# Kernel tuning notes

Measured on AMD Instinct MI355X. Metric: run time of the kernel, lower is better.

## Reference

```python
import jax, jax.numpy as jnp
import numpy as np

N_NODES = 50000
N_EDGES = 800000
NODE_DIM = 8
EDGE_DIM = 3
HIDDEN = 256
EMBED = 256
HEADS = 4
HEAD_DIM = HIDDEN // HEADS
LAYERS = 3
NUM_GRAPHS = 64
NEG_SLOPE = 0.2


def layer_norm(x, g, b, eps=1e-5):
    mu = jnp.mean(x, axis=-1, keepdims=True)
    var = jnp.var(x, axis=-1, keepdims=True)
    return (x - mu) * jax.lax.rsqrt(var + eps) * g + b


def setup_inputs() -> dict:
    key = jax.random.key(0)
    ks = jax.random.split(key, 20)
    s = lambda d: 1.0 / np.sqrt(d)
    inp = {
        "x": jax.random.normal(ks[0], (N_NODES, NODE_DIM), jnp.float32),
        "edge_index": jax.random.randint(ks[1], (2, N_EDGES), 0, N_NODES, jnp.int64),
        "edge_attr": jax.random.normal(ks[2], (N_EDGES, EDGE_DIM), jnp.float32),
        "batch": jnp.sort(jax.random.randint(ks[3], (N_NODES,), 0, NUM_GRAPHS, jnp.int64)),
        # input projection + LayerNorm
        "W_in": jax.random.normal(ks[4], (NODE_DIM, HIDDEN), jnp.float32) * s(NODE_DIM),
        "b_in": jnp.zeros((HIDDEN,), jnp.float32),
        "ln_in_g": jnp.ones((HIDDEN,), jnp.float32),
        "ln_in_b": jnp.zeros((HIDDEN,), jnp.float32),
        # stacked GAT layer params [LAYERS, ...]
        "W_gat": jax.random.normal(ks[5], (LAYERS, HIDDEN, HIDDEN), jnp.float32) * s(HIDDEN),
        "b_gat": jnp.zeros((LAYERS, HIDDEN), jnp.float32),
        "W_e": jax.random.normal(ks[6], (LAYERS, EDGE_DIM, HIDDEN), jnp.float32) * s(EDGE_DIM),
        "a_src": jax.random.normal(ks[7], (LAYERS, HEADS, HEAD_DIM), jnp.float32) * s(HEAD_DIM),
        "a_dst": jax.random.normal(ks[8], (LAYERS, HEADS, HEAD_DIM), jnp.float32) * s(HEAD_DIM),
        "a_edge": jax.random.normal(ks[9], (LAYERS, HEADS, HEAD_DIM), jnp.float32) * s(HEAD_DIM),
        # output projection + LayerNorm
        "W_out": jax.random.normal(ks[10], (EMBED, EMBED), jnp.float32) * s(EMBED),
        "b_out": jnp.zeros((EMBED,), jnp.float32),
        "ln_out_g": jnp.ones((EMBED,), jnp.float32),
        "ln_out_b": jnp.zeros((EMBED,), jnp.float32),
    }
    return inp


def gat_layer(h, src, dst, edge_attr, W, b, We, a_s, a_d, a_e):
    N = h.shape[0]
    hp = (h @ W + b).reshape(N, HEADS, HEAD_DIM)                 # [N,H,D]
    ep = (edge_attr @ We).reshape(-1, HEADS, HEAD_DIM)           # [E,H,D]
    hs = hp[src]                                                 # [E,H,D] gather
    hd = hp[dst]
    logit = (hs * a_s).sum(-1) + (hd * a_d).sum(-1) + (ep * a_e).sum(-1)  # [E,H]
    logit = jax.nn.leaky_relu(logit, NEG_SLOPE)
    # segment softmax over incoming edges per destination node
    m = jax.ops.segment_max(logit, dst, num_segments=N)          # [N,H]
    m = jnp.where(jnp.isfinite(m), m, 0.0)
    ex = jnp.exp(logit - m[dst])
    denom = jax.ops.segment_sum(ex, dst, num_segments=N)         # [N,H]
    alpha = ex / jnp.maximum(denom[dst], 1e-16)                  # [E,H]
    msg = hs * alpha[:, :, None]                                 # [E,H,D]
    out = jax.ops.segment_sum(msg, dst, num_segments=N).reshape(N, HIDDEN)
    return jax.nn.elu(out + h)                                   # residual + activation


def reference(x, edge_index, edge_attr, batch, W_in, b_in, ln_in_g, ln_in_b,
              W_gat, b_gat, W_e, a_src, a_dst, a_edge,
              W_out, b_out, ln_out_g, ln_out_b):
    src, dst = edge_index[0], edge_index[1]
    h = jax.nn.elu(layer_norm(x @ W_in + b_in, ln_in_g, ln_in_b))
    for l in range(LAYERS):
        h = gat_layer(h, src, dst, edge_attr,
                      W_gat[l], b_gat[l], W_e[l], a_src[l], a_dst[l], a_edge[l])
    node_emb = jax.nn.elu(layer_norm(h @ W_out + b_out, ln_out_g, ln_out_b))
    # global mean pool per graph
    sums = jax.ops.segment_sum(node_emb, batch, num_segments=NUM_GRAPHS)
    cnt = jax.ops.segment_sum(jnp.ones((node_emb.shape[0],), node_emb.dtype), batch,
                              num_segments=NUM_GRAPHS)
    graph_emb = sums / jnp.maximum(cnt, 1.0)[:, None]
    return graph_emb, node_emb
```

## Files before the change

### kernel.cpp

```cpp
#include <hip/hip_runtime.h>
#include <math.h>

#define HIDDEN 256
#define HEADS 4
#define HEAD_DIM 64
#define LAYERS 3
#define NUM_GRAPHS 64
#define NEG_SLOPE 0.2f

typedef short short8 __attribute__((ext_vector_type(8)));
typedef float floatx4 __attribute__((ext_vector_type(4)));

static __device__ __forceinline__ float elu_f(float x) {
    return x > 0.f ? x : expm1f(x);
}

static __device__ __forceinline__ float waveReduceSum(float v) {
#pragma unroll
    for (int off = 32; off > 0; off >>= 1) v += __shfl_xor(v, off, 64);
    return v;
}

static __device__ __forceinline__ ushort f2bf(float f) {
    unsigned u = __float_as_uint(f);
    unsigned r = (u + 0x7FFFu + ((u >> 16) & 1u)) >> 16;
    return (ushort)r;
}
static __device__ __forceinline__ float bf2f(ushort h) {
    return __uint_as_float(((unsigned)h) << 16);
}

__global__ void hist_kernel(const int* __restrict__ dst, int* __restrict__ deg, int E) {
    int e = blockIdx.x * blockDim.x + threadIdx.x;
    if (e < E) atomicAdd(&deg[dst[e]], 1);
}

__global__ __launch_bounds__(256) void blocksum_kernel(const int* __restrict__ deg,
                                                       int* __restrict__ bsum, int N) {
    int i = blockIdx.x * 256 + threadIdx.x;
    int v = (i < N) ? deg[i] : 0;
    __shared__ int red[4];
    int s = v;
#pragma unroll
    for (int off = 32; off > 0; off >>= 1) s += __shfl_xor(s, off, 64);
    if ((threadIdx.x & 63) == 0) red[threadIdx.x >> 6] = s;
    __syncthreads();
    if (threadIdx.x == 0) bsum[blockIdx.x] = red[0] + red[1] + red[2] + red[3];
}

__global__ __launch_bounds__(256) void scan_bsums(int* __restrict__ bsum, int nblk) {
    __shared__ int sh[256];
    int t = threadIdx.x;
    int v = (t < nblk) ? bsum[t] : 0;
    sh[t] = v;
    __syncthreads();
#pragma unroll
    for (int off = 1; off < 256; off <<= 1) {
        int add = (t >= off) ? sh[t - off] : 0;
        __syncthreads();
        sh[t] += add;
        __syncthreads();
    }
    if (t < nblk) bsum[t] = sh[t] - v;
}

__global__ __launch_bounds__(256) void writeptr_kernel(const int* __restrict__ deg,
                                                       const int* __restrict__ bsum,
                                                       int* __restrict__ rowptr,
                                                       int* __restrict__ nxt,
                                                       int N, int E) {
    __shared__ int sh[256];
    int t = threadIdx.x;
    int i = blockIdx.x * 256 + t;
    int v = (i < N) ? deg[i] : 0;
    sh[t] = v;
    __syncthreads();
#pragma unroll
    for (int off = 1; off < 256; off <<= 1) {
        int add = (t >= off) ? sh[t - off] : 0;
        __syncthreads();
        sh[t] += add;
        __syncthreads();
    }
    if (i < N) {
        int r = bsum[blockIdx.x] + sh[t] - v;
        rowptr[i] = r;
        nxt[i] = r;
    }
    if (i == 0) rowptr[N] = E;
}

__global__ void scatter_kernel(const int* __restrict__ src, const int* __restrict__ dst,
                               const float* __restrict__ ea, const float* __restrict__ wea,
                               int* __restrict__ nxt, int* __restrict__ smeta,
                               float* __restrict__ esc0, float* __restrict__ esc1,
                               float* __restrict__ esc2, int E) {
    int e = blockIdx.x * blockDim.x + threadIdx.x;
    if (e >= E) return;
    int d = dst[e];
    int slot = atomicAdd(&nxt[d], 1);
    smeta[slot] = src[e];
    float e0 = ea[(size_t)e * 3], e1 = ea[(size_t)e * 3 + 1], e2 = ea[(size_t)e * 3 + 2];
    float* escs[3] = {esc0, esc1, esc2};
#pragma unroll
    for (int l = 0; l < 3; ++l) {
        float4 v;
        float* vp = (float*)&v;
#pragma unroll
        for (int h = 0; h < 4; ++h) {
            const float* w = wea + l * 12 + h * 3;
            vp[h] = e0 * w[0] + e1 * w[1] + e2 * w[2];
        }
        *(float4*)(escs[l] + (size_t)slot * 4) = v;
    }
}

__global__ void wea_kernel(const float* __restrict__ We, const float* __restrict__ a_e,
                           float* __restrict__ w_ea) {
    int t = threadIdx.x;
    if (t < LAYERS * HEADS * 3) {
        int l = t / 12, r = t % 12, h = r / 3, k = r % 3;
        float s = 0.f;
        for (int d = 0; d < HEAD_DIM; ++d)
            s += We[l * 3 * HIDDEN + k * HIDDEN + h * HEAD_DIM + d] *
                 a_e[l * HIDDEN + h * HEAD_DIM + d];
        w_ea[t] = s;
    }
}

__global__ void conv_w(const float* __restrict__ Wg, const float* __restrict__ Wo,
                       ushort* __restrict__ Wt) {
    int l = blockIdx.x;
    int n = blockIdx.y;
    int k = threadIdx.x;
    const float* W = (l < 3) ? (Wg + (size_t)l * HIDDEN * HIDDEN) : Wo;
    Wt[(size_t)l * HIDDEN * HIDDEN + (size_t)n * HIDDEN + k] =
        f2bf(W[(size_t)k * HIDDEN + n]);
}

__global__ __launch_bounds__(256) void inproj_ln(const float* __restrict__ x,
                                                 const float* __restrict__ W,
                                                 const float* __restrict__ b,
                                                 const float* __restrict__ g,
                                                 const float* __restrict__ beta,
                                                 float* __restrict__ h,
                                                 ushort* __restrict__ hb) {
    int n = blockIdx.x;
    int c = threadIdx.x;
    float acc = b[c];
#pragma unroll
    for (int k = 0; k < 8; ++k) acc += x[n * 8 + k] * W[k * HIDDEN + c];
    __shared__ float red[8];
    float s = waveReduceSum(acc);
    float s2 = waveReduceSum(acc * acc);
    int w = c >> 6;
    if ((c & 63) == 0) { red[w] = s; red[4 + w] = s2; }
    __syncthreads();
    float mu = (red[0] + red[1] + red[2] + red[3]) * (1.f / 256.f);
    float ms = (red[4] + red[5] + red[6] + red[7]) * (1.f / 256.f);
    float inv = rsqrtf(ms - mu * mu + 1e-5f);
    float y = elu_f((acc - mu) * inv * g[c] + beta[c]);
    h[(size_t)n * HIDDEN + c] = y;
    hb[(size_t)n * HIDDEN + c] = f2bf(y);
}

__global__ __launch_bounds__(256) void ln_elu(const float* __restrict__ t,
                                              const float* __restrict__ g,
                                              const float* __restrict__ beta,
                                              float* __restrict__ out) {
    int n = blockIdx.x;
    int c = threadIdx.x;
    float acc = t[(size_t)n * HIDDEN + c];
    __shared__ float red[8];
    float s = waveReduceSum(acc);
    float s2 = waveReduceSum(acc * acc);
    int w = c >> 6;
    if ((c & 63) == 0) { red[w] = s; red[4 + w] = s2; }
    __syncthreads();
    float mu = (red[0] + red[1] + red[2] + red[3]) * (1.f / 256.f);
    float ms = (red[4] + red[5] + red[6] + red[7]) * (1.f / 256.f);
    float inv = rsqrtf(ms - mu * mu + 1e-5f);
    float y = (acc - mu) * inv * g[c] + beta[c];
    out[(size_t)n * HIDDEN + c] = elu_f(y);
}

#define ASTR 40
__global__ __launch_bounds__(256) void gemm_mfma(const ushort* __restrict__ A,
                                                 const ushort* __restrict__ Bt,
                                                 const float* __restrict__ bias,
                                                 float* __restrict__ C32,
                                                 ushort* __restrict__ C16,
                                                 const float* __restrict__ a_s,
                                                 const float* __restrict__ a_d,
                                                 float* __restrict__ s_src,
                                                 float* __restrict__ s_dst,
                                                 int doScore) {
    const int K = 256;
    __shared__ ushort As[128 * ASTR];
    __shared__ ushort Bs[128 * ASTR];
    int m0 = blockIdx.x * 128;
    int n0 = blockIdx.y * 128;
    int t = threadIdx.x;
    int wave = t >> 6, lane = t & 63;
    int wr = wave >> 1, wc = wave & 1;
    int lrow = lane & 15;
    int quad = lane >> 4;
    floatx4 acc[4][4] = {};
    int r = t >> 2, q = t & 3;
    for (int k0 = 0; k0 < K; k0 += 32) {
        __syncthreads();
        *(uint4*)&As[(r) * ASTR + q * 8] =
            *(const uint4*)(A + (size_t)(m0 + r) * K + k0 + q * 8);
        *(uint4*)&As[(r + 64) * ASTR + q * 8] =
            *(const uint4*)(A + (size_t)(m0 + r + 64) * K + k0 + q * 8);
        *(uint4*)&Bs[(r) * ASTR + q * 8] =
            *(const uint4*)(Bt + (size_t)(n0 + r) * K + k0 + q * 8);
        *(uint4*)&Bs[(r + 64) * ASTR + q * 8] =
            *(const uint4*)(Bt + (size_t)(n0 + r + 64) * K + k0 + q * 8);
        __syncthreads();
        short8 af[4], bfr[4];
#pragma unroll
        for (int i = 0; i < 4; ++i)
            af[i] = *(const short8*)&As[(wr * 64 + i * 16 + lrow) * ASTR + quad * 8];
#pragma unroll
        for (int j = 0; j < 4; ++j)
            bfr[j] = *(const short8*)&Bs[(wc * 64 + j * 16 + lrow) * ASTR + quad * 8];
#pragma unroll
        for (int i = 0; i < 4; ++i)
#pragma unroll
            for (int j = 0; j < 4; ++j)
                acc[i][j] = __builtin_amdgcn_mfma_f32_16x16x32_bf16(af[i], bfr[j],
                                                                    acc[i][j], 0, 0, 0);
    }
    int hh = (n0 + wc * 64) >> 6;
    int ncol[4];
    float bv4[4], asv[4], adv[4];
#pragma unroll
    for (int j = 0; j < 4; ++j) {
        int n = n0 + wc * 64 + j * 16 + lrow;
        ncol[j] = n;
        bv4[j] = bias[n];
        asv[j] = a_s[n];
        adv[j] = a_d[n];
    }
#pragma unroll
    for (int i = 0; i < 4; ++i) {
#pragma unroll
        for (int rg = 0; rg < 4; ++rg) {
            int mrow = m0 + wr * 64 + i * 16 + quad * 4 + rg;
            float ps = 0.f, pd = 0.f;
#pragma unroll
            for (int j = 0; j < 4; ++j) {
                float v = acc[i][j][rg] + bv4[j];
                if (C32) C32[(size_t)mrow * HIDDEN + ncol[j]] = v;
                if (C16) C16[(size_t)mrow * HIDDEN + ncol[j]] = f2bf(v);
                ps = fmaf(v, asv[j], ps);
                pd = fmaf(v, adv[j], pd);
            }
            if (doScore) {
#pragma unroll
                for (int off = 1; off < 16; off <<= 1) {
                    ps += __shfl_xor(ps, off, 64);
                    pd += __shfl_xor(pd, off, 64);
                }
                if (lrow == 0) {
                    s_src[mrow * 4 + hh] = ps;
                    s_dst[mrow * 4 + hh] = pd;
                }
            }
        }
    }
}

__global__ __launch_bounds__(256) void aggregate(const int* __restrict__ rowptr,
                                                 const int* __restrict__ smeta,
                                                 const float* __restrict__ escl,
                                                 const float* __restrict__ s_src,
                                                 const float* __restrict__ s_dst,
                                                 const ushort* __restrict__ hpb,
                                                 const float* __restrict__ h_in,
                                                 float* __restrict__ h_out,
                                                 ushort* __restrict__ h_out_bf,
                                                 int N) {
    int wv = threadIdx.x >> 6;
    int n = blockIdx.x * 4 + wv;
    if (n >= N) return;
    int l = threadIdx.x & 63;
    int h = l >> 4;
    int e4 = l & 15;
    int c0 = l * 4;
    float sdn = s_dst[n * 4 + h];
    int beg = rowptr[n];
    int cnt = rowptr[n + 1] - beg;
    float m = -3e38f, dsum = 0.f, a0 = 0.f, a1 = 0.f, a2 = 0.f, a3 = 0.f;
    for (int ch = 0; ch < cnt; ch += 16) {
        int i = ch + e4;
        int s = 0;
        float lg = -3e38f;
        if (i < cnt) {
            s = smeta[beg + i];
            float tv = sdn + s_src[s * 4 + h] + escl[(size_t)(beg + i) * 4 + h];
            lg = tv > 0.f ? tv : NEG_SLOPE * tv;
        }
        float cm = lg;
#pragma unroll
        for (int off = 1; off < 16; off <<= 1)
            cm = fmaxf(cm, __shfl_xor(cm, off, 64));
        float mn = fmaxf(m, cm);
        float scl = __expf(m - mn);
        m = mn;
        dsum *= scl; a0 *= scl; a1 *= scl; a2 *= scl; a3 *= scl;
        float ex = __expf(lg - mn);
        int lim = min(16, cnt - ch);
#pragma unroll 4
        for (int j = 0; j < lim; ++j) {
            float exj = __shfl(ex, (h << 4) | j, 64);
            int sj = __shfl(s, j, 64);
            uint2 v = *(const uint2*)(hpb + (size_t)sj * HIDDEN + c0);
            dsum += exj;
            float f0 = __uint_as_float(v.x << 16);
            float f1 = __uint_as_float(v.x & 0xFFFF0000u);
            float f2 = __uint_as_float(v.y << 16);
            float f3 = __uint_as_float(v.y & 0xFFFF0000u);
            a0 = fmaf(f0, exj, a0);
            a1 = fmaf(f1, exj, a1);
            a2 = fmaf(f2, exj, a2);
            a3 = fmaf(f3, exj, a3);
        }
    }
    float inv = 1.f / fmaxf(dsum, 1e-16f);
    float4 hi = *(const float4*)(h_in + (size_t)n * HIDDEN + c0);
    float y0 = elu_f(fmaf(a0, inv, hi.x));
    float y1 = elu_f(fmaf(a1, inv, hi.y));
    float y2 = elu_f(fmaf(a2, inv, hi.z));
    float y3 = elu_f(fmaf(a3, inv, hi.w));
    float4 yo = {y0, y1, y2, y3};
    *(float4*)(h_out + (size_t)n * HIDDEN + c0) = yo;
    ushort4 yb = {f2bf(y0), f2bf(y1), f2bf(y2), f2bf(y3)};
    *(ushort4*)(h_out_bf + (size_t)n * HIDDEN + c0) = yb;
}

__global__ __launch_bounds__(256) void pool_partial(const float* __restrict__ nemb,
                                                    const int* __restrict__ batch,
                                                    float* __restrict__ gout, int N) {
    int r0 = blockIdx.x * 128;
    int c = threadIdx.x;
    __shared__ int bsh[128];
    if (c < 128) {
        int r = r0 + c;
        bsh[c] = (r < N) ? batch[r] : -1;
    }
    __syncthreads();
    int rend = min(128, N - r0);
    float acc = 0.f;
    int cur = bsh[0];
    for (int i = 0; i < rend; ++i) {
        int g = bsh[i];
        if (g != cur) {
            atomicAdd(&gout[cur * HIDDEN + c], acc);
            acc = 0.f;
            cur = g;
        }
        acc += nemb[(size_t)(r0 + i) * HIDDEN + c];
    }
    if (cur >= 0) atomicAdd(&gout[cur * HIDDEN + c], acc);
}

__global__ void pool_div(float* __restrict__ gout, const int* __restrict__ batch, int N) {
    int g = blockIdx.x;
    int c = threadIdx.x;
    int lo = 0, hi = N;
    while (lo < hi) { int mid = (lo + hi) >> 1; if (batch[mid] < g) lo = mid + 1; else hi = mid; }
    int start = lo;
    lo = start; hi = N;
    while (lo < hi) { int mid = (lo + hi) >> 1; if (batch[mid] < g + 1) lo = mid + 1; else hi = mid; }
    float cnt = (float)(lo - start);
    gout[g * HIDDEN + c] /= fmaxf(cnt, 1.f);
}

extern "C" void kernel_launch(void* const* d_in, const int* in_sizes, int n_in,
                              void* d_out, int out_size, void* d_ws, size_t ws_size,
                              hipStream_t stream) {
    const float* x       = (const float*)d_in[0];
    const int*   ei      = (const int*)d_in[1];
    const float* ea      = (const float*)d_in[2];
    const int*   batch   = (const int*)d_in[3];
    const float* W_in    = (const float*)d_in[4];
    const float* b_in    = (const float*)d_in[5];
    const float* ln_in_g = (const float*)d_in[6];
    const float* ln_in_b = (const float*)d_in[7];
    const float* W_gat   = (const float*)d_in[8];
    const float* b_gat   = (const float*)d_in[9];
    const float* W_e     = (const float*)d_in[10];
    const float* a_src   = (const float*)d_in[11];
    const float* a_dst   = (const float*)d_in[12];
    const float* a_edge  = (const float*)d_in[13];
    const float* W_out   = (const float*)d_in[14];
    const float* b_out   = (const float*)d_in[15];
    const float* ln_out_g= (const float*)d_in[16];
    const float* ln_out_b= (const float*)d_in[17];

    int N = in_sizes[0] / 8;
    int E = in_sizes[1] / 2;
    int Mpad = (N + 127) & ~127;
    int nblk = (N + 255) / 256;
    const int* srcA = ei;
    const int* dstA = ei + E;

    char* w = (char*)d_ws;
    size_t off = 0;
    auto alloc = [&](size_t bytes) {
        void* p = w + off;
        off += (bytes + 255) & ~(size_t)255;
        return p;
    };
    float*    hA     = (float*)alloc((size_t)Mpad * HIDDEN * 4);
    float*    hB     = (float*)alloc((size_t)Mpad * HIDDEN * 4);
    ushort*   hAb    = (ushort*)alloc((size_t)Mpad * HIDDEN * 2);
    ushort*   hBb    = (ushort*)alloc((size_t)Mpad * HIDDEN * 2);
    ushort*   hpb    = (ushort*)alloc((size_t)Mpad * HIDDEN * 2);
    float*    sSrc   = (float*)alloc((size_t)Mpad * 4 * 4);
    float*    sDst   = (float*)alloc((size_t)Mpad * 4 * 4);
    int*      deg    = (int*)alloc((size_t)N * 4);
    int*      rowptr = (int*)alloc((size_t)(N + 1) * 4);
    int*      nxt    = (int*)alloc((size_t)N * 4);
    int*      bsum   = (int*)alloc(256 * 4);
    int*      smeta  = (int*)alloc((size_t)E * 4);
    float*    esc0   = (float*)alloc((size_t)E * 4 * 4);
    float*    esc1   = (float*)alloc((size_t)E * 4 * 4);
    float*    esc2   = (float*)alloc((size_t)E * 4 * 4);
    float*    wea    = (float*)alloc(64 * 4);
    ushort*   Wt     = (ushort*)alloc((size_t)4 * HIDDEN * HIDDEN * 2);
    float*    escs[3] = {esc0, esc1, esc2};

    hipMemsetAsync(deg, 0, (size_t)N * 4, stream);
    hist_kernel<<<(E + 255) / 256, 256, 0, stream>>>(dstA, deg, E);
    blocksum_kernel<<<nblk, 256, 0, stream>>>(deg, bsum, N);
    scan_bsums<<<1, 256, 0, stream>>>(bsum, nblk);
    writeptr_kernel<<<nblk, 256, 0, stream>>>(deg, bsum, rowptr, nxt, N, E);
    wea_kernel<<<1, 64, 0, stream>>>(W_e, a_edge, wea);
    scatter_kernel<<<(E + 255) / 256, 256, 0, stream>>>(srcA, dstA, ea, wea, nxt,
                                                        smeta, esc0, esc1, esc2, E);
    conv_w<<<dim3(4, HIDDEN), 256, 0, stream>>>(W_gat, W_out, Wt);

    inproj_ln<<<N, 256, 0, stream>>>(x, W_in, b_in, ln_in_g, ln_in_b, hA, hAb);

    float* hcur = hA;   ushort* hcurb = hAb;
    float* hnext = hB;  ushort* hnextb = hBb;
    dim3 gg(Mpad / 128, HIDDEN / 128);
    for (int l = 0; l < LAYERS; ++l) {
        gemm_mfma<<<gg, 256, 0, stream>>>(hcurb, Wt + (size_t)l * HIDDEN * HIDDEN,
                                          b_gat + l * HIDDEN, nullptr, hpb,
                                          a_src + l * HIDDEN, a_dst + l * HIDDEN,
                                          sSrc, sDst, 1);
        aggregate<<<(N + 3) / 4, 256, 0, stream>>>(rowptr, smeta, escs[l], sSrc, sDst,
                                                   hpb, hcur, hnext, hnextb, N);
        float* tf = hcur; hcur = hnext; hnext = tf;
        ushort* tb = hcurb; hcurb = hnextb; hnextb = tb;
    }

    float* hp32 = hnext;
    gemm_mfma<<<gg, 256, 0, stream>>>(hcurb, Wt + (size_t)3 * HIDDEN * HIDDEN,
                                      b_out, hp32, nullptr, a_src, a_dst, sSrc, sDst, 0);
    float* gout = (float*)d_out;
    float* nemb = gout + (size_t)NUM_GRAPHS * HIDDEN;
    ln_elu<<<N, 256, 0, stream>>>(hp32, ln_out_g, ln_out_b, nemb);
    hipMemsetAsync(gout, 0, (size_t)NUM_GRAPHS * HIDDEN * 4, stream);
    pool_partial<<<(N + 127) / 128, 256, 0, stream>>>(nemb, batch, gout, N);
    pool_div<<<NUM_GRAPHS, 256, 0, stream>>>(gout, batch, N);
}
```

Measured before the change: 749.5 us.

## Pack edge metadata and recompute edge scores; register-prefetch GEMM tiles

The scatter kernel now writes one packed 16-byte record per edge (source index plus three raw edge attributes) instead of a source index and three per-layer score arrays. Each aggregate call recomputes the per-head edge score from those attributes and the layer's folded edge weights. This cuts scatter write traffic, though aggregate now reads 16 bytes per edge instead of 4+4 (a slot in a 16-byte record). Separately, the GEMM prefetches the next K-slice into registers while the current slice is computed, overlapping global loads with MFMA work at the cost of extra registers.

```diff
diff --git a/kernel.cpp b/kernel.cpp
--- a/kernel.cpp
+++ b/kernel.cpp
@@ -91,28 +91,18 @@
 }
 
 __global__ void scatter_kernel(const int* __restrict__ src, const int* __restrict__ dst,
-                               const float* __restrict__ ea, const float* __restrict__ wea,
-                               int* __restrict__ nxt, int* __restrict__ smeta,
-                               float* __restrict__ esc0, float* __restrict__ esc1,
-                               float* __restrict__ esc2, int E) {
+                               const float* __restrict__ ea,
+                               int* __restrict__ nxt, uint4* __restrict__ emeta, int E) {
     int e = blockIdx.x * blockDim.x + threadIdx.x;
     if (e >= E) return;
     int d = dst[e];
     int slot = atomicAdd(&nxt[d], 1);
-    smeta[slot] = src[e];
-    float e0 = ea[(size_t)e * 3], e1 = ea[(size_t)e * 3 + 1], e2 = ea[(size_t)e * 3 + 2];
-    float* escs[3] = {esc0, esc1, esc2};
-#pragma unroll
-    for (int l = 0; l < 3; ++l) {
-        float4 v;
-        float* vp = (float*)&v;
-#pragma unroll
-        for (int h = 0; h < 4; ++h) {
-            const float* w = wea + l * 12 + h * 3;
-            vp[h] = e0 * w[0] + e1 * w[1] + e2 * w[2];
-        }
-        *(float4*)(escs[l] + (size_t)slot * 4) = v;
-    }
+    uint4 mt;
+    mt.x = (unsigned)src[e];
+    mt.y = __float_as_uint(ea[(size_t)e * 3]);
+    mt.z = __float_as_uint(ea[(size_t)e * 3 + 1]);
+    mt.w = __float_as_uint(ea[(size_t)e * 3 + 2]);
+    emeta[slot] = mt;
 }
 
 __global__ void wea_kernel(const float* __restrict__ We, const float* __restrict__ a_e,
@@ -207,17 +197,26 @@
     int quad = lane >> 4;
     floatx4 acc[4][4] = {};
     int r = t >> 2, q = t & 3;
+    const ushort* Ar0 = A + (size_t)(m0 + r) * K + q * 8;
+    const ushort* Ar1 = A + (size_t)(m0 + r + 64) * K + q * 8;
+    const ushort* Br0 = Bt + (size_t)(n0 + r) * K + q * 8;
+    const ushort* Br1 = Bt + (size_t)(n0 + r + 64) * K + q * 8;
+    uint4 ra0 = *(const uint4*)(Ar0);
+    uint4 ra1 = *(const uint4*)(Ar1);
+    uint4 rb0 = *(const uint4*)(Br0);
+    uint4 rb1 = *(const uint4*)(Br1);
     for (int k0 = 0; k0 < K; k0 += 32) {
-        __syncthreads();
-        *(uint4*)&As[(r) * ASTR + q * 8] =
-            *(const uint4*)(A + (size_t)(m0 + r) * K + k0 + q * 8);
-        *(uint4*)&As[(r + 64) * ASTR + q * 8] =
-            *(const uint4*)(A + (size_t)(m0 + r + 64) * K + k0 + q * 8);
-        *(uint4*)&Bs[(r) * ASTR + q * 8] =
-            *(const uint4*)(Bt + (size_t)(n0 + r) * K + k0 + q * 8);
-        *(uint4*)&Bs[(r + 64) * ASTR + q * 8] =
-            *(const uint4*)(Bt + (size_t)(n0 + r + 64) * K + k0 + q * 8);
-        __syncthreads();
+        *(uint4*)&As[(r) * ASTR + q * 8] = ra0;
+        *(uint4*)&As[(r + 64) * ASTR + q * 8] = ra1;
+        *(uint4*)&Bs[(r) * ASTR + q * 8] = rb0;
+        *(uint4*)&Bs[(r + 64) * ASTR + q * 8] = rb1;
+        __syncthreads();
+        if (k0 + 32 < K) {
+            ra0 = *(const uint4*)(Ar0 + k0 + 32);
+            ra1 = *(const uint4*)(Ar1 + k0 + 32);
+            rb0 = *(const uint4*)(Br0 + k0 + 32);
+            rb1 = *(const uint4*)(Br1 + k0 + 32);
+        }
         short8 af[4], bfr[4];
 #pragma unroll
         for (int i = 0; i < 4; ++i)
@@ -231,6 +230,7 @@
             for (int j = 0; j < 4; ++j)
                 acc[i][j] = __builtin_amdgcn_mfma_f32_16x16x32_bf16(af[i], bfr[j],
                                                                     acc[i][j], 0, 0, 0);
+        __syncthreads();
     }
     int hh = (n0 + wc * 64) >> 6;
     int ncol[4];
@@ -273,8 +273,8 @@
 }
 
 __global__ __launch_bounds__(256) void aggregate(const int* __restrict__ rowptr,
-                                                 const int* __restrict__ smeta,
-                                                 const float* __restrict__ escl,
+                                                 const uint4* __restrict__ emeta,
+                                                 const float* __restrict__ wea_l,
                                                  const float* __restrict__ s_src,
                                                  const float* __restrict__ s_dst,
                                                  const ushort* __restrict__ hpb,
@@ -289,6 +289,7 @@
     int h = l >> 4;
     int e4 = l & 15;
     int c0 = l * 4;
+    float w0 = wea_l[h * 3], w1 = wea_l[h * 3 + 1], w2 = wea_l[h * 3 + 2];
     float sdn = s_dst[n * 4 + h];
     int beg = rowptr[n];
     int cnt = rowptr[n + 1] - beg;
@@ -298,8 +299,11 @@
         int s = 0;
         float lg = -3e38f;
         if (i < cnt) {
-            s = smeta[beg + i];
-            float tv = sdn + s_src[s * 4 + h] + escl[(size_t)(beg + i) * 4 + h];
+            uint4 mt = emeta[beg + i];
+            s = (int)mt.x;
+            float esc = __uint_as_float(mt.y) * w0 + __uint_as_float(mt.z) * w1 +
+                        __uint_as_float(mt.w) * w2;
+            float tv = sdn + s_src[s * 4 + h] + esc;
             lg = tv > 0.f ? tv : NEG_SLOPE * tv;
         }
         float cm = lg;
@@ -425,13 +429,9 @@
     int*      rowptr = (int*)alloc((size_t)(N + 1) * 4);
     int*      nxt    = (int*)alloc((size_t)N * 4);
     int*      bsum   = (int*)alloc(256 * 4);
-    int*      smeta  = (int*)alloc((size_t)E * 4);
-    float*    esc0   = (float*)alloc((size_t)E * 4 * 4);
-    float*    esc1   = (float*)alloc((size_t)E * 4 * 4);
-    float*    esc2   = (float*)alloc((size_t)E * 4 * 4);
+    uint4*    emeta  = (uint4*)alloc((size_t)E * 16);
     float*    wea    = (float*)alloc(64 * 4);
     ushort*   Wt     = (ushort*)alloc((size_t)4 * HIDDEN * HIDDEN * 2);
-    float*    escs[3] = {esc0, esc1, esc2};
 
     hipMemsetAsync(deg, 0, (size_t)N * 4, stream);
     hist_kernel<<<(E + 255) / 256, 256, 0, stream>>>(dstA, deg, E);
@@ -439,8 +439,7 @@
     scan_bsums<<<1, 256, 0, stream>>>(bsum, nblk);
     writeptr_kernel<<<nblk, 256, 0, stream>>>(deg, bsum, rowptr, nxt, N, E);
     wea_kernel<<<1, 64, 0, stream>>>(W_e, a_edge, wea);
-    scatter_kernel<<<(E + 255) / 256, 256, 0, stream>>>(srcA, dstA, ea, wea, nxt,
-                                                        smeta, esc0, esc1, esc2, E);
+    scatter_kernel<<<(E + 255) / 256, 256, 0, stream>>>(srcA, dstA, ea, nxt, emeta, E);
     conv_w<<<dim3(4, HIDDEN), 256, 0, stream>>>(W_gat, W_out, Wt);
 
     inproj_ln<<<N, 256, 0, stream>>>(x, W_in, b_in, ln_in_g, ln_in_b, hA, hAb);
@@ -453,8 +452,9 @@
                                           b_gat + l * HIDDEN, nullptr, hpb,
                                           a_src + l * HIDDEN, a_dst + l * HIDDEN,
                                           sSrc, sDst, 1);
-        aggregate<<<(N + 3) / 4, 256, 0, stream>>>(rowptr, smeta, escs[l], sSrc, sDst,
-                                                   hpb, hcur, hnext, hnextb, N);
+        aggregate<<<(N + 3) / 4, 256, 0, stream>>>(rowptr, emeta, wea + l * 12,
+                                                   sSrc, sDst, hpb, hcur, hnext,
+                                                   hnextb, N);
         float* tf = hcur; hcur = hnext; hnext = tf;
         ushort* tb = hcurb; hcurb = hnextb; hnextb = tb;
     }
```

Result: faster. 688.0 us (-8.2%).
